# Optimization experiments

Measured on AMD Instinct MI355X. Metric: run time of the kernel, lower is better.

The kernel has to match this reference:

```python
import jax, jax.numpy as jnp
import numpy as np

NEG = -1e30       # log-space 'zero'
KD_FACTOR = 0.5   # self.kd_factor
KD_TEMP = 1.0     # self.kd_temp is never set in the original __init__; use 1.0
BLANK = 0         # torch CTCLoss default blank id


def ctc_loss(logits, targets, ilens, olens):
    """CTC negative log-likelihood, sum-reduced / B (matches builtin path:
    log_softmax + nn.CTCLoss(reduction='sum', zero_infinity=True) / batch).
    logits: [B,T,C]; targets: [B,L] label ids (no blanks); ilens, olens: [B]."""
    B, T, C = logits.shape
    L = targets.shape[1]
    S = 2 * L + 1
    lp = jax.nn.log_softmax(logits, axis=-1)                     # [B,T,C]
    # extended label sequence: blank, y1, blank, y2, ..., blank  -> [B,S]
    ext = jnp.zeros((B, S), dtype=targets.dtype).at[:, 1::2].set(targets)
    prev2 = jnp.pad(ext, ((0, 0), (2, 0)))[:, :S]
    allow2 = (ext != BLANK) & (ext != prev2) & (jnp.arange(S)[None, :] >= 2)
    # per-frame emission log-probs of extended labels: [T,B,S]
    emit = jnp.take_along_axis(lp, jnp.broadcast_to(ext[:, None, :], (B, T, S)), axis=2)
    emit = jnp.transpose(emit, (1, 0, 2))
    alpha0 = (jnp.full((B, S), NEG, dtype=lp.dtype)
              .at[:, 0].set(emit[0, :, 0])
              .at[:, 1].set(emit[0, :, 1]))

    def step(alpha, xs):
        e_t, t = xs
        s1 = jnp.pad(alpha, ((0, 0), (1, 0)), constant_values=NEG)[:, :S]
        s2 = jnp.where(allow2, jnp.pad(alpha, ((0, 0), (2, 0)), constant_values=NEG)[:, :S], NEG)
        m = jnp.maximum(jnp.maximum(alpha, s1), s2)
        new = m + jnp.log(jnp.exp(alpha - m) + jnp.exp(s1 - m) + jnp.exp(s2 - m)) + e_t
        # freeze alpha past each sample's input length -> alpha at t = ilen-1
        new = jnp.where((t < ilens)[:, None], new, alpha)
        return new, None

    alpha, _ = jax.lax.scan(step, alpha0, (emit[1:], jnp.arange(1, T)))
    end = 2 * olens                                              # last blank index
    bidx = jnp.arange(B)
    ll = jnp.logaddexp(alpha[bidx, end], alpha[bidx, end - 1])
    loss = -ll
    loss = jnp.where(loss > 1e20, 0.0, loss)                     # zero_infinity
    return loss.sum() / B


def kd_loss(logits, soft_logits, hlens):
    """Vectorized form of the per-sample ragged KD loop:
    sum_b -(softmax(soft[b,:h]/T) * log_softmax(logits[b,:h]/T)).sum() / B."""
    B, T, _ = logits.shape
    p = jax.nn.softmax(soft_logits / KD_TEMP, axis=-1)
    logq = jax.nn.log_softmax(logits / KD_TEMP, axis=-1)
    cxe = -(p * logq).sum(-1)                                    # [B,T]
    mask = jnp.arange(T)[None, :] < hlens[:, None]
    return jnp.where(mask, cxe, 0.0).sum() / B


def setup_inputs() -> dict:
    key = jax.random.key(0)
    k1, k2, k3, k4, k5, k6 = jax.random.split(key, 6)
    B, T, E, V, L = 16, 512, 512, 5000, 64
    hs_pad = jax.random.normal(k1, (B, T, E), jnp.float32)
    soft_logits = jax.random.normal(k2, (B, T, V), jnp.float32)
    W = jax.random.normal(k3, (E, V), jnp.float32) * 0.02
    b = jnp.zeros((V,), jnp.float32)
    hlens = jax.random.randint(k4, (B,), 300, T + 1)             # T >= 2L+1 guaranteed
    targets = jax.random.randint(k5, (B, L), 1, V)               # no blank labels
    olens = jax.random.randint(k6, (B,), 32, L + 1)
    return {"hs_pad": hs_pad, "soft_logits": soft_logits, "W": W, "b": b,
            "hlens": hlens, "targets": targets, "olens": olens}


def reference(hs_pad, soft_logits, W, b, hlens, targets, olens):
    # ctc_lo(F.dropout(hs_pad, p=0.0)) -> plain linear projection
    logits = hs_pad @ W + b                                      # [B,T,V]
    loss_ctc = ctc_loss(logits, targets, hlens, olens)
    loss_kd = kd_loss(logits, soft_logits, hlens)
    return KD_FACTOR * loss_kd + (1.0 - KD_FACTOR) * loss_ctc
```

## Files before the change

### kernel.cpp

```cpp
#include <hip/hip_runtime.h>
#include <math.h>

#define LOG2E 1.4426950408889634f
#define LN2 0.6931471805599453f

constexpr int B_ = 16;
constexpr int T_ = 512;
constexpr int E_ = 512;
constexpr int V_ = 5000;
constexpr int VP_ = 5120;
constexpr int L_ = 64;
constexpr int S_ = 2 * L_ + 1;
constexpr int SP_ = 132;

typedef __attribute__((ext_vector_type(8))) short bf16x8;
typedef __attribute__((ext_vector_type(4))) float f32x4;

#define GLOAD_LDS16(g, l)                                                              \
  __builtin_amdgcn_global_load_lds((const __attribute__((address_space(1))) void*)(g), \
                                   (__attribute__((address_space(3))) void*)(l), 16, 0, 0)

__device__ __forceinline__ unsigned short f2bf(float x) {
  unsigned int u = __float_as_uint(x);
  unsigned int r = (u + 0x7fffu + ((u >> 16) & 1u)) >> 16;
  return (unsigned short)r;
}
__device__ __forceinline__ float bf2f(unsigned int lo16) {
  return __uint_as_float(lo16 << 16);
}

__device__ __forceinline__ float hexp2(float x) { return __builtin_amdgcn_exp2f(x); }
__device__ __forceinline__ float hlog2(float x) { return __builtin_amdgcn_logf(x); }

__device__ __forceinline__ float dpp_shr1_zero(float v) {
  int s = __float_as_int(v);
  int bc = __builtin_amdgcn_update_dpp(0, s, 0x142, 0xF, 0xF, false);
  int r = __builtin_amdgcn_update_dpp(bc, s, 0x111, 0xF, 0xF, false);
  return __int_as_float(r);
}

template <int CTRL>
__device__ __forceinline__ float dpp_mv(float v) {
  int s = __float_as_int(v);
  return __int_as_float(__builtin_amdgcn_update_dpp(s, s, CTRL, 0xF, 0xF, false));
}

__device__ __forceinline__ float blockReduceF(float v, bool is_max, volatile float* red) {
  int tid = threadIdx.x, lane = tid & 63, wid = tid >> 6;
#pragma unroll
  for (int off = 32; off > 0; off >>= 1) {
    float o = __shfl_down(v, off, 64);
    v = is_max ? fmaxf(v, o) : (v + o);
  }
  __syncthreads();
  if (lane == 0) red[wid] = v;
  __syncthreads();
  float r = red[0];
#pragma unroll
  for (int w = 1; w < 4; ++w) r = is_max ? fmaxf(r, (float)red[w]) : (r + (float)red[w]);
  return r;
}

__global__ __launch_bounds__(256) void convA(const float* __restrict__ X,
                                             unsigned short* __restrict__ Y, int n4) {
  int i = blockIdx.x * 256 + threadIdx.x;
  if (i >= n4) return;
  float4 v = ((const float4*)X)[i];
  ushort4 o;
  o.x = f2bf(v.x); o.y = f2bf(v.y); o.z = f2bf(v.z); o.w = f2bf(v.w);
  ((ushort4*)Y)[i] = o;
}

__global__ __launch_bounds__(256) void convW(const float* __restrict__ W,
                                             unsigned short* __restrict__ Wt) {
  __shared__ float tile[32][33];
  int n0 = blockIdx.x * 32, k0 = blockIdx.y * 32;
  int tid = threadIdx.x;
  int tx = tid & 31, ty = tid >> 5;
#pragma unroll
  for (int p = 0; p < 4; ++p) {
    int k = k0 + ty + p * 8, n = n0 + tx;
    tile[ty + p * 8][tx] = (n < V_) ? W[(size_t)k * V_ + n] : 0.0f;
  }
  __syncthreads();
#pragma unroll
  for (int p = 0; p < 4; ++p) {
    int n = n0 + ty + p * 8, k = k0 + tx;
    Wt[(size_t)n * E_ + k] = f2bf(tile[tx][ty + p * 8]);
  }
}

__global__ __launch_bounds__(256) void gemm_mfma(const unsigned short* __restrict__ A,
                                                 const unsigned short* __restrict__ Wt,
                                                 const float* __restrict__ bias,
                                                 unsigned short* __restrict__ C) {
  __shared__ unsigned short As[128 * 32];
  __shared__ unsigned short Bs[128 * 32];
  int tid = threadIdx.x;
  int l = tid & 63, wid = tid >> 6;
  int lane15 = l & 15, lhalf = l >> 4;
  int wr = wid >> 1, wc = wid & 1;
  int bm = blockIdx.y * 128;
  int bn = blockIdx.x * 128;

  f32x4 acc[4][4] = {};

  int srow = l >> 2;
  int scol = (((l & 3) ^ ((l >> 3) & 3)) << 3);
  int rswz = ((lhalf ^ ((lane15 >> 1) & 3)) << 3);
  for (int k0 = 0; k0 < E_; k0 += 32) {
#pragma unroll
    for (int i = 0; i < 2; ++i) {
      int rb = wid * 32 + i * 16;
      GLOAD_LDS16(A + (size_t)(bm + rb + srow) * E_ + k0 + scol, &As[rb * 32]);
      GLOAD_LDS16(Wt + (size_t)(bn + rb + srow) * E_ + k0 + scol, &Bs[rb * 32]);
    }
    __syncthreads();
    bf16x8 af[4], bf[4];
#pragma unroll
    for (int m = 0; m < 4; ++m)
      af[m] = *(const bf16x8*)&As[(wr * 64 + m * 16 + lane15) * 32 + rswz];
#pragma unroll
    for (int n = 0; n < 4; ++n)
      bf[n] = *(const bf16x8*)&Bs[(wc * 64 + n * 16 + lane15) * 32 + rswz];
#pragma unroll
    for (int m = 0; m < 4; ++m)
#pragma unroll
      for (int n = 0; n < 4; ++n)
        acc[m][n] = __builtin_amdgcn_mfma_f32_16x16x32_bf16(af[m], bf[n], acc[m][n], 0, 0, 0);
    __syncthreads();
  }

#pragma unroll
  for (int n = 0; n < 4; ++n) {
    int col = bn + wc * 64 + n * 16 + lane15;
    float bv = (col < V_) ? bias[col] : 0.0f;
#pragma unroll
    for (int m = 0; m < 4; ++m) {
      int row0 = bm + wr * 64 + m * 16 + lhalf * 4;
#pragma unroll
      for (int j = 0; j < 4; ++j) {
        C[(size_t)(row0 + j) * VP_ + col] = f2bf(acc[m][n][j] + bv);
      }
    }
  }
}

__global__ __launch_bounds__(256) void row_fused(const unsigned short* __restrict__ Cc,
                                                 const float* __restrict__ soft,
                                                 const int* __restrict__ hlens,
                                                 const int* __restrict__ targets,
                                                 float* __restrict__ cxe,
                                                 float* __restrict__ emit, int r0) {
  int r = blockIdx.x;
  int row = r0 + r;
  int bidx = row >> 9;
  int t = row & (T_ - 1);
  const unsigned short* crow = Cc + (size_t)r * VP_;
  const uint4* lrow = (const uint4*)crow;
  const float4* srow = (const float4*)(soft + (size_t)row * V_);
  __shared__ float red[4];
  int tid = threadIdx.x;

  uint4 lu[3];
  float4 sv[3][2];
  bool valid[3];
#pragma unroll
  for (int k = 0; k < 3; ++k) {
    int slot = tid + k * 256;
    valid[k] = (slot < V_ / 8);
    if (valid[k]) {
      lu[k] = lrow[slot];
      sv[k][0] = srow[slot * 2];
      sv[k][1] = srow[slot * 2 + 1];
    }
  }

  float maxl = -INFINITY, maxs = -INFINITY;
#pragma unroll
  for (int k = 0; k < 3; ++k) {
    if (valid[k]) {
      unsigned int w0 = lu[k].x, w1 = lu[k].y, w2 = lu[k].z, w3 = lu[k].w;
      maxl = fmaxf(maxl, fmaxf(fmaxf(bf2f(w0 & 0xffffu), bf2f(w0 >> 16)),
                               fmaxf(bf2f(w1 & 0xffffu), bf2f(w1 >> 16))));
      maxl = fmaxf(maxl, fmaxf(fmaxf(bf2f(w2 & 0xffffu), bf2f(w2 >> 16)),
                               fmaxf(bf2f(w3 & 0xffffu), bf2f(w3 >> 16))));
      float4 a = sv[k][0], b = sv[k][1];
      maxs = fmaxf(maxs, fmaxf(fmaxf(a.x, a.y), fmaxf(a.z, a.w)));
      maxs = fmaxf(maxs, fmaxf(fmaxf(b.x, b.y), fmaxf(b.z, b.w)));
    }
  }
  maxl = blockReduceF(maxl, true, red);
  maxs = blockReduceF(maxs, true, red);

  float suml = 0.f, sums = 0.f, dot = 0.f;
#pragma unroll
  for (int k = 0; k < 3; ++k) {
    if (valid[k]) {
      float lv[8], ss[8];
      unsigned int w0 = lu[k].x, w1 = lu[k].y, w2 = lu[k].z, w3 = lu[k].w;
      lv[0] = bf2f(w0 & 0xffffu); lv[1] = bf2f(w0 >> 16);
      lv[2] = bf2f(w1 & 0xffffu); lv[3] = bf2f(w1 >> 16);
      lv[4] = bf2f(w2 & 0xffffu); lv[5] = bf2f(w2 >> 16);
      lv[6] = bf2f(w3 & 0xffffu); lv[7] = bf2f(w3 >> 16);
      float4 a = sv[k][0], b = sv[k][1];
      ss[0] = a.x; ss[1] = a.y; ss[2] = a.z; ss[3] = a.w;
      ss[4] = b.x; ss[5] = b.y; ss[6] = b.z; ss[7] = b.w;
#pragma unroll
      for (int j = 0; j < 8; ++j) {
        suml += hexp2((lv[j] - maxl) * LOG2E);
        float e = hexp2((ss[j] - maxs) * LOG2E);
        sums += e;
        dot = fmaf(e, lv[j], dot);
      }
    }
  }
  suml = blockReduceF(suml, false, red);
  sums = blockReduceF(sums, false, red);
  dot = blockReduceF(dot, false, red);

  float lse = maxl + hlog2(suml) * LN2;
  if (tid == 0) {
    cxe[row] = (t < hlens[bidx]) ? (lse - dot / sums) : 0.0f;
  }

  if (tid < 64) {
    int i0 = tid, i1 = tid + 64;
    int idx0 = (i0 & 1) ? targets[bidx * L_ + (i0 >> 1)] : 0;
    int idx1 = (i1 & 1) ? targets[bidx * L_ + (i1 >> 1)] : 0;
    float e0 = (bf2f(crow[idx0]) - lse) * LOG2E;
    float e1 = (bf2f(crow[idx1]) - lse) * LOG2E;
    float e2 = 0.f;
    if (tid == 0) e2 = (bf2f(crow[0]) - lse) * LOG2E;
    float m = fmaxf(e0, e1);
    if (tid == 0) m = fmaxf(m, e2);
#pragma unroll
    for (int off = 32; off > 0; off >>= 1) m = fmaxf(m, __shfl_xor(m, off, 64));
    float* erow = emit + ((size_t)bidx * T_ + t) * SP_;
    erow[i0] = hexp2(e0 - m);
    erow[i1] = hexp2(e1 - m);
    if (tid == 0) {
      erow[128] = hexp2(e2 - m);
      erow[130] = m;
    }
  }
}

__device__ __forceinline__ void pstep(float& a0, float& a1, float& a2, float allowf,
                                      float e0, float e1, float e2) {
  float ua1 = dpp_shr1_zero(a1);
  float n0 = (a0 + ua1) * e0;
  float n1 = fmaf(ua1, allowf, a0 + a1) * e1;
  float n2 = (a2 + a1) * e2;
  a0 = n0; a1 = n1; a2 = n2;
}

__device__ __forceinline__ void renorm(float& a0, float& a1, float& a2, float& shift,
                                       int lane) {
  float m = fmaxf(a0, a1);
  m = (lane == 63) ? fmaxf(m, a2) : m;
  m = fmaxf(m, dpp_mv<0xB1>(m));
  m = fmaxf(m, dpp_mv<0x4E>(m));
  m = fmaxf(m, dpp_mv<0x124>(m));
  m = fmaxf(m, dpp_mv<0x128>(m));
  m = fmaxf(m, __shfl_xor(m, 16, 64));
  m = fmaxf(m, __shfl_xor(m, 32, 64));
  m = fmaxf(m, 1e-35f);
  float rs = __builtin_amdgcn_rcpf(m) * 281474976710656.0f;
  a0 *= rs; a1 *= rs; a2 *= rs;
  shift -= hlog2(rs);
}

__global__ __launch_bounds__(64) void ctc_fwd(const float* __restrict__ emit,
                                              const int* __restrict__ hlens,
                                              const int* __restrict__ targets,
                                              const int* __restrict__ olens,
                                              float* __restrict__ ctc_out) {
  int b = blockIdx.x;
  int l = threadIdx.x;
  const float* Eb = emit + (size_t)b * T_ * SP_;
  float allowf = 0.f;
  if (l >= 1) allowf = (targets[b * L_ + l] != targets[b * L_ + l - 1]) ? 1.0f : 0.0f;

  float a0, a1, a2, shift;
  {
    float2 e01 = *(const float2*)(Eb + 2 * l);
    float4 x = *(const float4*)(Eb + 128);
    a0 = (l == 0) ? e01.x : 0.0f;
    a1 = (l == 0) ? e01.y : 0.0f;
    a2 = 0.0f;
    shift = x.z;
  }
  int ilen = hlens[b];

#define LDE(tt) (*(const float2*)(Eb + (size_t)(tt) * SP_ + 2 * l))
#define LDX(tt) (*(const float4*)(Eb + (size_t)(tt) * SP_ + 128))

  float2 c0 = LDE(1), c1 = LDE(2), c2 = LDE(3), c3 = LDE(4);
  float2 c4 = LDE(5), c5 = LDE(6), c6 = LDE(7), c7 = LDE(8);
  float4 x0 = LDX(1), x1 = LDX(2), x2 = LDX(3), x3 = LDX(4);
  float4 x4 = LDX(5), x5 = LDX(6), x6 = LDX(7), x7 = LDX(8);

  int t = 1;
  for (; t + 7 <= ilen - 1; t += 8) {
    float2 p0 = LDE(t + 8), p1 = LDE(t + 9), p2 = LDE(t + 10), p3 = LDE(t + 11);
    float2 p4 = LDE(t + 12), p5 = LDE(t + 13), p6 = LDE(t + 14), p7 = LDE(t + 15);
    float4 q0 = LDX(t + 8), q1 = LDX(t + 9), q2 = LDX(t + 10), q3 = LDX(t + 11);
    float4 q4 = LDX(t + 12), q5 = LDX(t + 13), q6 = LDX(t + 14), q7 = LDX(t + 15);
    pstep(a0, a1, a2, allowf, c0.x, c0.y, x0.x);
    pstep(a0, a1, a2, allowf, c1.x, c1.y, x1.x);
    pstep(a0, a1, a2, allowf, c2.x, c2.y, x2.x);
    pstep(a0, a1, a2, allowf, c3.x, c3.y, x3.x);
    pstep(a0, a1, a2, allowf, c4.x, c4.y, x4.x);
    pstep(a0, a1, a2, allowf, c5.x, c5.y, x5.x);
    pstep(a0, a1, a2, allowf, c6.x, c6.y, x6.x);
    pstep(a0, a1, a2, allowf, c7.x, c7.y, x7.x);
    shift += ((x0.z + x1.z) + (x2.z + x3.z)) + ((x4.z + x5.z) + (x6.z + x7.z));
    renorm(a0, a1, a2, shift, l);
    c0 = p0; c1 = p1; c2 = p2; c3 = p3; c4 = p4; c5 = p5; c6 = p6; c7 = p7;
    x0 = q0; x1 = q1; x2 = q2; x3 = q3; x4 = q4; x5 = q5; x6 = q6; x7 = q7;
  }
  int rem = ilen - t;
  if (rem > 0) { pstep(a0, a1, a2, allowf, c0.x, c0.y, x0.x); shift += x0.z; }
  if (rem > 1) { pstep(a0, a1, a2, allowf, c1.x, c1.y, x1.x); shift += x1.z; }
  if (rem > 2) { pstep(a0, a1, a2, allowf, c2.x, c2.y, x2.x); shift += x2.z; }
  if (rem > 3) { pstep(a0, a1, a2, allowf, c3.x, c3.y, x3.x); shift += x3.z; }
  if (rem > 4) { pstep(a0, a1, a2, allowf, c4.x, c4.y, x4.x); shift += x4.z; }
  if (rem > 5) { pstep(a0, a1, a2, allowf, c5.x, c5.y, x5.x); shift += x5.z; }
  if (rem > 6) { pstep(a0, a1, a2, allowf, c6.x, c6.y, x6.x); shift += x6.z; }
#undef LDE
#undef LDX

  int end = 2 * olens[b];
  float aE = (end == 128) ? __shfl(a2, 63, 64) : __shfl(a0, end >> 1, 64);
  float aE1 = __shfl(a1, (end >> 1) - 1, 64);
  if (l == 0) {
    float p = aE + aE1;
    float ll = (hlog2(p) + shift) * LN2;
    float loss = -ll;
    if (!(loss <= 1e20f)) loss = 0.0f;
    ctc_out[b] = loss;
  }
}

__global__ __launch_bounds__(256) void final_reduce(const float* __restrict__ cxe,
                                                    const float* __restrict__ ctco,
                                                    float* __restrict__ out) {
  __shared__ float red[4];
  float s = 0.f;
  for (int i = threadIdx.x; i < B_ * T_; i += 256) s += cxe[i];
  s = blockReduceF(s, false, red);
  if (threadIdx.x == 0) {
    float c = 0.f;
    for (int b = 0; b < B_; ++b) c += ctco[b];
    out[0] = 0.5f * (s / (float)B_) + 0.5f * (c / (float)B_);
  }
}

extern "C" void kernel_launch(void* const* d_in, const int* in_sizes, int n_in,
                              void* d_out, int out_size, void* d_ws, size_t ws_size,
                              hipStream_t stream) {
  const float* hs = (const float*)d_in[0];
  const float* soft = (const float*)d_in[1];
  const float* W = (const float*)d_in[2];
  const float* bias = (const float*)d_in[3];
  const int* hlens = (const int*)d_in[4];
  const int* targets = (const int*)d_in[5];
  const int* olens = (const int*)d_in[6];
  float* out = (float*)d_out;

  int total = B_ * T_;
  size_t emit_n = (size_t)(total + 16) * SP_;
  float* emit = (float*)d_ws;
  float* cxe = emit + emit_n;
  float* ctco = cxe + (size_t)total;
  unsigned short* Abf = (unsigned short*)(ctco + 16);
  unsigned short* Wt = Abf + (size_t)total * E_;
  unsigned short* logits = Wt + (size_t)VP_ * E_;
  size_t used = (size_t)((char*)logits - (char*)d_ws);
  size_t avail = (ws_size > used) ? (ws_size - used) : 0;
  int max_rows = (int)(avail / ((size_t)VP_ * sizeof(unsigned short)));
  int chunk = max_rows & ~127;
  if (chunk > total) chunk = total;
  if (chunk < 128) chunk = 128;

  dim3 blk(256);
  {
    int n4 = total * E_ / 4;
    hipLaunchKernelGGL(convA, dim3((n4 + 255) / 256), blk, 0, stream, hs, Abf, n4);
    hipLaunchKernelGGL(convW, dim3(VP_ / 32, E_ / 32), blk, 0, stream, W, Wt);
  }

  for (int r0 = 0; r0 < total; r0 += chunk) {
    int mc = total - r0;
    if (mc > chunk) mc = chunk;
    dim3 g1(VP_ / 128, mc / 128);
    hipLaunchKernelGGL(gemm_mfma, g1, blk, 0, stream, Abf + (size_t)r0 * E_, Wt, bias, logits);
    hipLaunchKernelGGL(row_fused, dim3(mc), blk, 0, stream, logits, soft, hlens, targets,
                       cxe, emit, r0);
  }
  hipLaunchKernelGGL(ctc_fwd, dim3(B_), dim3(64), 0, stream, emit, hlens, targets, olens, ctco);
  hipLaunchKernelGGL(final_reduce, dim3(1), blk, 0, stream, cxe, ctco, out);
}
```

Baseline: 178.5 us.

## Skip padded frames past hlens in GEMM and row kernel; deepen GEMM K-tile

The GEMM now exits early for 128-row tiles that lie entirely beyond the sample's input length. In partially valid tiles it only stores rows with t < hlen. The row-fused kernel returns immediately for padded frames after writing a zero KD term, so it no longer reads the large soft-logit rows or computes emissions for them. Separately, the GEMM K-step grows from 32 to 64 with a new LDS swizzle, halving the number of barrier pairs at the cost of twice the shared memory. Correctness relies on the CTC forward never reading emit rows past hlen.

```diff
diff --git a/kernel.cpp b/kernel.cpp
--- a/kernel.cpp
+++ b/kernel.cpp
@@ -93,41 +93,64 @@
 __global__ __launch_bounds__(256) void gemm_mfma(const unsigned short* __restrict__ A,
                                                  const unsigned short* __restrict__ Wt,
                                                  const float* __restrict__ bias,
-                                                 unsigned short* __restrict__ C) {
-  __shared__ unsigned short As[128 * 32];
-  __shared__ unsigned short Bs[128 * 32];
+                                                 const int* __restrict__ hlens,
+                                                 unsigned short* __restrict__ C, int r0) {
+  __shared__ unsigned short As[128 * 64];
+  __shared__ unsigned short Bs[128 * 64];
   int tid = threadIdx.x;
   int l = tid & 63, wid = tid >> 6;
   int lane15 = l & 15, lhalf = l >> 4;
   int wr = wid >> 1, wc = wid & 1;
   int bm = blockIdx.y * 128;
   int bn = blockIdx.x * 128;
+  int bmAbs = r0 + bm;
+  int hl = hlens[bmAbs >> 9];
+  int tIn = bmAbs & (T_ - 1);
+  if (tIn >= hl) return;
 
   f32x4 acc[4][4] = {};
 
-  int srow = l >> 2;
-  int scol = (((l & 3) ^ ((l >> 3) & 3)) << 3);
-  int rswz = ((lhalf ^ ((lane15 >> 1) & 3)) << 3);
-  for (int k0 = 0; k0 < E_; k0 += 32) {
-#pragma unroll
-    for (int i = 0; i < 2; ++i) {
-      int rb = wid * 32 + i * 16;
-      GLOAD_LDS16(A + (size_t)(bm + rb + srow) * E_ + k0 + scol, &As[rb * 32]);
-      GLOAD_LDS16(Wt + (size_t)(bn + rb + srow) * E_ + k0 + scol, &Bs[rb * 32]);
+  int srow = l >> 3;
+  int scol = (((l & 7) ^ srow) << 3);
+  int rsw0 = ((lhalf ^ (lane15 & 7)) << 3);
+  int rsw1 = (((4 + lhalf) ^ (lane15 & 7)) << 3);
+#pragma unroll
+  for (int k0 = 0; k0 < E_; k0 += 64) {
+#pragma unroll
+    for (int i = 0; i < 4; ++i) {
+      int rb = wid * 32 + i * 8;
+      GLOAD_LDS16(A + (size_t)(bm + rb + srow) * E_ + k0 + scol, &As[rb * 64]);
+      GLOAD_LDS16(Wt + (size_t)(bn + rb + srow) * E_ + k0 + scol, &Bs[rb * 64]);
     }
     __syncthreads();
-    bf16x8 af[4], bf[4];
-#pragma unroll
-    for (int m = 0; m < 4; ++m)
-      af[m] = *(const bf16x8*)&As[(wr * 64 + m * 16 + lane15) * 32 + rswz];
-#pragma unroll
-    for (int n = 0; n < 4; ++n)
-      bf[n] = *(const bf16x8*)&Bs[(wc * 64 + n * 16 + lane15) * 32 + rswz];
-#pragma unroll
-    for (int m = 0; m < 4; ++m)
+    {
+      bf16x8 af[4], bf[4];
+#pragma unroll
+      for (int m = 0; m < 4; ++m)
+        af[m] = *(const bf16x8*)&As[(wr * 64 + m * 16 + lane15) * 64 + rsw0];
 #pragma unroll
       for (int n = 0; n < 4; ++n)
-        acc[m][n] = __builtin_amdgcn_mfma_f32_16x16x32_bf16(af[m], bf[n], acc[m][n], 0, 0, 0);
+        bf[n] = *(const bf16x8*)&Bs[(wc * 64 + n * 16 + lane15) * 64 + rsw0];
+#pragma unroll
+      for (int m = 0; m < 4; ++m)
+#pragma unroll
+        for (int n = 0; n < 4; ++n)
+          acc[m][n] = __builtin_amdgcn_mfma_f32_16x16x32_bf16(af[m], bf[n], acc[m][n], 0, 0, 0);
+    }
+    {
+      bf16x8 af[4], bf[4];
+#pragma unroll
+      for (int m = 0; m < 4; ++m)
+        af[m] = *(const bf16x8*)&As[(wr * 64 + m * 16 + lane15) * 64 + rsw1];
+#pragma unroll
+      for (int n = 0; n < 4; ++n)
+        bf[n] = *(const bf16x8*)&Bs[(wc * 64 + n * 16 + lane15) * 64 + rsw1];
+#pragma unroll
+      for (int m = 0; m < 4; ++m)
+#pragma unroll
+        for (int n = 0; n < 4; ++n)
+          acc[m][n] = __builtin_amdgcn_mfma_f32_16x16x32_bf16(af[m], bf[n], acc[m][n], 0, 0, 0);
+    }
     __syncthreads();
   }
 
@@ -137,10 +160,11 @@
     float bv = (col < V_) ? bias[col] : 0.0f;
 #pragma unroll
     for (int m = 0; m < 4; ++m) {
-      int row0 = bm + wr * 64 + m * 16 + lhalf * 4;
+      int rloc = wr * 64 + m * 16 + lhalf * 4;
 #pragma unroll
       for (int j = 0; j < 4; ++j) {
-        C[(size_t)(row0 + j) * VP_ + col] = f2bf(acc[m][n][j] + bv);
+        if (tIn + rloc + j < hl)
+          C[(size_t)(bm + rloc + j) * VP_ + col] = f2bf(acc[m][n][j] + bv);
       }
     }
   }
@@ -156,11 +180,16 @@
   int row = r0 + r;
   int bidx = row >> 9;
   int t = row & (T_ - 1);
+  int tid = threadIdx.x;
+  int hl = hlens[bidx];
+  if (t >= hl) {
+    if (tid == 0) cxe[row] = 0.0f;
+    return;
+  }
   const unsigned short* crow = Cc + (size_t)r * VP_;
   const uint4* lrow = (const uint4*)crow;
   const float4* srow = (const float4*)(soft + (size_t)row * V_);
   __shared__ float red[4];
-  int tid = threadIdx.x;
 
   uint4 lu[3];
   float4 sv[3][2];
@@ -221,7 +250,7 @@
 
   float lse = maxl + hlog2(suml) * LN2;
   if (tid == 0) {
-    cxe[row] = (t < hlens[bidx]) ? (lse - dot / sums) : 0.0f;
+    cxe[row] = lse - dot / sums;
   }
 
   if (tid < 64) {
@@ -395,7 +424,8 @@
     int mc = total - r0;
     if (mc > chunk) mc = chunk;
     dim3 g1(VP_ / 128, mc / 128);
-    hipLaunchKernelGGL(gemm_mfma, g1, blk, 0, stream, Abf + (size_t)r0 * E_, Wt, bias, logits);
+    hipLaunchKernelGGL(gemm_mfma, g1, blk, 0, stream, Abf + (size_t)r0 * E_, Wt, bias,
+                       hlens, logits, r0);
     hipLaunchKernelGGL(row_fused, dim3(mc), blk, 0, stream, logits, soft, hlens, targets,
                        cxe, emit, r0);
   }
```

Measured after the change: 180.8 us. No clear change (+1.3%).
